# Performance work log

Hardware: AMD Instinct MI355X
Metric: run time of the kernel (lower is better)

## Reference

```python
import jax, jax.numpy as jnp
import numpy as np

N = 50000      # num nodes
NE = 20000     # num hyperedges
NNZ = 1000000  # incidence pairs |{(v,e)}|
F_IN = 128
HID = 64
NCLS = 40
NLAYER = 4
ALPHA = 0.1    # args.restart_alpha
LAMDA = 0.5


def setup_inputs() -> dict:
    key = jax.random.key(0)
    ks = jax.random.split(key, 8)
    x = jax.random.normal(ks[0], (N, F_IN), dtype=jnp.float32)
    vertex = jax.random.randint(ks[1], (NNZ,), 0, N, dtype=jnp.int32)
    edges = jax.random.randint(ks[2], (NNZ,), 0, NE, dtype=jnp.int32)
    W0 = jax.random.normal(ks[3], (F_IN, HID), dtype=jnp.float32) / np.float32(np.sqrt(F_IN))
    b0 = jnp.zeros((HID,), jnp.float32)
    Ws = jax.random.normal(ks[4], (NLAYER, HID, HID), dtype=jnp.float32) / np.float32(np.sqrt(HID))
    Wout = jax.random.normal(ks[5], (HID, NCLS), dtype=jnp.float32) / np.float32(np.sqrt(HID))
    bout = jnp.zeros((NCLS,), jnp.float32)
    return {"x": x, "vertex": vertex, "edges": edges, "W0": W0, "b0": b0,
            "Ws": Ws, "Wout": Wout, "bout": bout}


def _scatter_mean(src, idx, num_segments):
    s = jax.ops.segment_sum(src, idx, num_segments=num_segments)
    cnt = jax.ops.segment_sum(jnp.ones((idx.shape[0],), src.dtype), idx, num_segments=num_segments)
    return s / jnp.maximum(cnt, 1.0)[:, None]


def _normalize_l2(X):
    # torch: rownorm = X.detach().norm(dim=1, keepdim=True); scale = rownorm^-1; inf->0
    norm = jax.lax.stop_gradient(jnp.sqrt(jnp.sum(X * X, axis=-1, keepdims=True)))
    scale = jnp.where(norm > 0, 1.0 / jnp.maximum(norm, jnp.float32(1e-30)), 0.0)
    return X * scale


def reference(x, vertex, edges, W0, b0, Ws, Wout, bout):
    # input linear + relu (dropout = identity in eval mode)
    X = jax.nn.relu(x @ W0 + b0)
    X0 = X
    for i in range(NLAYER):
        beta = float(np.log(LAMDA / (i + 1) + 1.0))
        Xve = X[vertex]                       # gather node -> incidence  [NNZ, HID]
        Xe = _scatter_mean(Xve, edges, NE)    # scatter-mean -> hyperedge [NE, HID]
        Xev = Xe[edges]                       # gather hyperedge -> incidence [NNZ, HID]
        Xv = _scatter_mean(Xev, vertex, N)    # scatter-mean -> node      [N, HID]
        Xv = _normalize_l2(Xv)                # args.UniGNN_use_norm = True
        Xi = (1.0 - ALPHA) * Xv + ALPHA * X0
        X = jax.nn.relu((1.0 - beta) * Xi + beta * (Xi @ Ws[i]))
    return X @ Wout + bout
```

## Files before the change

### kernel.cpp

```cpp
#include <hip/hip_runtime.h>
#include <hip/hip_fp16.h>
#include <math.h>

#define N_NODES 50000
#define N_EDGES 20000
#define NNZ_C   1000000
#define F_IN    128
#define HID     64
#define NCLS    40
#define NLAYER  4
#define ALPHA   0.1f

#define ESHIFT  6
#define VSHIFT  7
#define NB_E    ((N_EDGES + 63) / 64)
#define NB_V    ((N_NODES + 127) / 128)
#define NB_TOT  (NB_E + NB_V)

typedef _Float16 f16x8 __attribute__((ext_vector_type(8)));
typedef float    f32x4 __attribute__((ext_vector_type(4)));

__global__ __launch_bounds__(256) void input_gemm(
    const float* __restrict__ x, const float* __restrict__ W0,
    const float* __restrict__ b0, _Float16* __restrict__ X0h)
{
    int lane = threadIdx.x & 63;
    int wv   = threadIdx.x >> 6;
    int r16  = lane & 15;
    int kgrp = lane >> 4;
    f16x8 bf[4][4];
    #pragma unroll
    for (int n0 = 0; n0 < 4; ++n0)
        #pragma unroll
        for (int kh = 0; kh < 4; ++kh)
            #pragma unroll
            for (int j = 0; j < 8; ++j)
                bf[n0][kh][j] = (_Float16)W0[(kh * 32 + kgrp * 8 + j) * HID + n0 * 16 + r16];
    float bias[4];
    #pragma unroll
    for (int n0 = 0; n0 < 4; ++n0) bias[n0] = b0[n0 * 16 + r16];

    int nwaves = gridDim.x * 4;
    for (int t = blockIdx.x * 4 + wv; t < N_NODES / 16; t += nwaves) {
        int row0 = t * 16;
        const float* xp = x + (size_t)(row0 + r16) * F_IN + kgrp * 8;
        f16x8 a[4];
        #pragma unroll
        for (int kh = 0; kh < 4; ++kh) {
            float4 u0 = *(const float4*)(xp + kh * 32);
            float4 u1 = *(const float4*)(xp + kh * 32 + 4);
            a[kh][0] = (_Float16)u0.x; a[kh][1] = (_Float16)u0.y;
            a[kh][2] = (_Float16)u0.z; a[kh][3] = (_Float16)u0.w;
            a[kh][4] = (_Float16)u1.x; a[kh][5] = (_Float16)u1.y;
            a[kh][6] = (_Float16)u1.z; a[kh][7] = (_Float16)u1.w;
        }
        #pragma unroll
        for (int n0 = 0; n0 < 4; ++n0) {
            f32x4 acc = {0.f, 0.f, 0.f, 0.f};
            #pragma unroll
            for (int kh = 0; kh < 4; ++kh)
                acc = __builtin_amdgcn_mfma_f32_16x16x32_f16(a[kh], bf[n0][kh], acc, 0, 0, 0);
            #pragma unroll
            for (int r = 0; r < 4; ++r) {
                float y = acc[r] + bias[n0];
                y = y > 0.f ? y : 0.f;
                X0h[(size_t)(row0 + kgrp * 4 + r) * HID + n0 * 16 + r16] = (_Float16)y;
            }
        }
    }
}

__global__ __launch_bounds__(256) void make_wp(
    const float* __restrict__ Ws, _Float16* __restrict__ Wp,
    float be0, float be1, float be2, float be3)
{
    int l = blockIdx.x;
    float beta = (l == 0) ? be0 : (l == 1) ? be1 : (l == 2) ? be2 : be3;
    for (int i = threadIdx.x; i < HID * HID; i += 256) {
        int k = i >> 6, n = i & 63;
        float v = beta * Ws[l * HID * HID + i] + ((k == n) ? (1.f - beta) : 0.f);
        Wp[l * HID * HID + i] = (_Float16)v;
    }
}

__global__ __launch_bounds__(256) void bucket_hist(
    const int* __restrict__ vertex, const int* __restrict__ edges,
    int* __restrict__ gcnt)
{
    __shared__ int h[NB_TOT];
    int tid = threadIdx.x;
    for (int i = tid; i < NB_TOT; i += 256) h[i] = 0;
    __syncthreads();
    int base = blockIdx.x * 4096;
    int n = NNZ_C - base; if (n > 4096) n = 4096;
    for (int i = tid * 4; i < n; i += 1024) {
        int4 e4 = *(const int4*)(edges  + base + i);
        int4 v4 = *(const int4*)(vertex + base + i);
        atomicAdd(&h[e4.x >> ESHIFT], 1);
        atomicAdd(&h[e4.y >> ESHIFT], 1);
        atomicAdd(&h[e4.z >> ESHIFT], 1);
        atomicAdd(&h[e4.w >> ESHIFT], 1);
        atomicAdd(&h[NB_E + (v4.x >> VSHIFT)], 1);
        atomicAdd(&h[NB_E + (v4.y >> VSHIFT)], 1);
        atomicAdd(&h[NB_E + (v4.z >> VSHIFT)], 1);
        atomicAdd(&h[NB_E + (v4.w >> VSHIFT)], 1);
    }
    __syncthreads();
    for (int i = tid; i < NB_TOT; i += 256)
        if (h[i]) atomicAdd(&gcnt[i], h[i]);
}

__global__ __launch_bounds__(1024) void bucket_scan(
    const int* __restrict__ gcnt, int* __restrict__ boff_e,
    int* __restrict__ boff_v, int* __restrict__ curb)
{
    __shared__ int tmp[1024];
    int tid = threadIdx.x;
    int v = (tid < NB_TOT) ? gcnt[tid] : 0;
    tmp[tid] = v;
    __syncthreads();
    for (int d = 1; d < 1024; d <<= 1) {
        int t = (tid >= d) ? tmp[tid - d] : 0;
        __syncthreads();
        tmp[tid] += t;
        __syncthreads();
    }
    if (tid < NB_TOT) {
        int excl = tmp[tid] - v;
        int off = (tid < NB_E) ? excl : excl - NNZ_C;
        if (tid < NB_E) boff_e[tid] = off; else boff_v[tid - NB_E] = off;
        curb[tid] = off;
    }
    if (tid == 0) { boff_e[NB_E] = NNZ_C; boff_v[NB_V] = NNZ_C; }
}

__global__ __launch_bounds__(256) void bin_pass1_both(
    const int* __restrict__ vertex, const int* __restrict__ edges,
    int* __restrict__ curb,
    unsigned* __restrict__ binned_e,
    unsigned* __restrict__ binned_v)
{
    __shared__ int hist[NB_TOT];
    __shared__ int base[NB_TOT];
    int tid = threadIdx.x;
    int blk = blockIdx.x * 4096;
    int nh = NNZ_C - blk; if (nh > 4096) nh = 4096;
    int ee[16], vv[16];
    int nche = 0;
    #pragma unroll
    for (int k = 0; k < 4; ++k) {
        int i = tid * 4 + k * 1024;
        if (i < nh) {
            int4 e4 = *(const int4*)(edges  + blk + i);
            int4 v4 = *(const int4*)(vertex + blk + i);
            ee[k*4+0]=e4.x; ee[k*4+1]=e4.y; ee[k*4+2]=e4.z; ee[k*4+3]=e4.w;
            vv[k*4+0]=v4.x; vv[k*4+1]=v4.y; vv[k*4+2]=v4.z; vv[k*4+3]=v4.w;
            nche = k + 1;
        }
    }
    for (int i = tid; i < NB_TOT; i += 256) hist[i] = 0;
    __syncthreads();
    for (int k = 0; k < nche; ++k) {
        #pragma unroll
        for (int q = 0; q < 4; ++q) {
            atomicAdd(&hist[ee[k*4+q] >> ESHIFT], 1);
            atomicAdd(&hist[NB_E + (vv[k*4+q] >> VSHIFT)], 1);
        }
    }
    __syncthreads();
    for (int i = tid; i < NB_TOT; i += 256) {
        int c = hist[i];
        base[i] = c ? atomicAdd(&curb[i], c) : 0;
        hist[i] = 0;
    }
    __syncthreads();
    for (int k = 0; k < nche; ++k) {
        #pragma unroll
        for (int q = 0; q < 4; ++q) {
            int e = ee[k*4+q], v = vv[k*4+q];
            int be = e >> ESHIFT;
            int r  = atomicAdd(&hist[be], 1);
            binned_e[base[be] + r] = ((unsigned)e << 16) | (unsigned)v;
            int bv = NB_E + (v >> VSHIFT);
            int r2 = atomicAdd(&hist[bv], 1);
            binned_v[base[bv] + r2] = ((unsigned)v << 15) | (unsigned)e;
        }
    }
}

__global__ __launch_bounds__(256) void bin_pass2f(
    const unsigned* __restrict__ binned, const int* __restrict__ boff,
    int shift, int kshift, int nkeys,
    int* __restrict__ off, float* __restrict__ inv, int* __restrict__ adj)
{
    __shared__ int lcnt[128];
    __shared__ int ts[128];
    __shared__ int lcur[128];
    int b  = blockIdx.x;
    int k0 = b << shift;
    int bs = 1 << shift;
    int kn = nkeys - k0; if (kn > bs) kn = bs;
    int tid = threadIdx.x;
    unsigned vmask = (1u << kshift) - 1u;
    if (tid < 128) lcnt[tid] = 0;
    __syncthreads();
    int beg = boff[b], end = boff[b + 1];
    for (int j = beg + tid; j < end; j += 256)
        atomicAdd(&lcnt[(int)(binned[j] >> kshift) - k0], 1);
    __syncthreads();
    int c = 0;
    if (tid < 128) { c = lcnt[tid]; ts[tid] = c; }
    __syncthreads();
    #pragma unroll
    for (int d = 1; d < 128; d <<= 1) {
        int t = 0;
        if (tid < 128 && tid >= d) t = ts[tid - d];
        __syncthreads();
        if (tid < 128) ts[tid] += t;
        __syncthreads();
    }
    if (tid < kn) {
        int pos = beg + ts[tid] - c;
        off[k0 + tid] = pos;
        inv[k0 + tid] = 1.0f / fmaxf((float)c, 1.0f);
        lcur[tid] = pos;
    }
    if (b == 0 && tid == 0) off[nkeys] = NNZ_C;
    __syncthreads();
    for (int j = beg + tid; j < end; j += 256) {
        unsigned p = binned[j];
        int k = (int)(p >> kshift) - k0;
        int v = (int)(p & vmask);
        adj[atomicAdd(&lcur[k], 1)] = v;
    }
}

__device__ __forceinline__ void gather_rows(
    const __half* __restrict__ src, const int* __restrict__ adj,
    int beg, int end, int lane, float acc[8])
{
    int g = lane >> 3, c = lane & 7;
    for (int j = beg; j < end; j += 64) {
        int nj = end - j; if (nj > 64) nj = 64;
        int myidx = (lane < nj) ? adj[j + lane] : 0;
        int idx[8];
        #pragma unroll
        for (int s = 0; s < 8; ++s)
            idx[s] = __shfl(myidx, ((s << 3) + g) & 63);
        #pragma unroll
        for (int s = 0; s < 8; ++s) {
            int r = (s << 3) + g;
            if (r < nj) {
                uint4 raw = ((const uint4*)(src + (size_t)idx[s] * HID))[c];
                union { uint4 u; __half2 h[4]; } U; U.u = raw;
                float2 f0 = __half22float2(U.h[0]);
                float2 f1 = __half22float2(U.h[1]);
                float2 f2 = __half22float2(U.h[2]);
                float2 f3 = __half22float2(U.h[3]);
                acc[0] += f0.x; acc[1] += f0.y;
                acc[2] += f1.x; acc[3] += f1.y;
                acc[4] += f2.x; acc[5] += f2.y;
                acc[6] += f3.x; acc[7] += f3.y;
            }
        }
    }
    #pragma unroll
    for (int q = 0; q < 8; ++q) {
        acc[q] += __shfl_xor(acc[q], 8);
        acc[q] += __shfl_xor(acc[q], 16);
        acc[q] += __shfl_xor(acc[q], 32);
    }
}

__global__ __launch_bounds__(256) void edge_gather(
    const __half* __restrict__ Xh, const int* __restrict__ adj_e,
    const int* __restrict__ off_e, const float* __restrict__ inv_e,
    __half* __restrict__ Xeh)
{
    int wid  = blockIdx.x * 4 + (threadIdx.x >> 6);
    int lane = threadIdx.x & 63;
    float acc[8] = {0.f,0.f,0.f,0.f,0.f,0.f,0.f,0.f};
    gather_rows(Xh, adj_e, off_e[wid], off_e[wid + 1], lane, acc);
    if ((lane >> 3) == 0) {
        float sc = inv_e[wid];
        union { uint4 u; __half2 h[4]; } O;
        O.h[0] = __floats2half2_rn(acc[0] * sc, acc[1] * sc);
        O.h[1] = __floats2half2_rn(acc[2] * sc, acc[3] * sc);
        O.h[2] = __floats2half2_rn(acc[4] * sc, acc[5] * sc);
        O.h[3] = __floats2half2_rn(acc[6] * sc, acc[7] * sc);
        ((uint4*)(Xeh + (size_t)wid * HID))[lane] = O.u;
    }
}

__global__ __launch_bounds__(256) void node_gather(
    const __half* __restrict__ Xeh, const int* __restrict__ adj_v,
    const int* __restrict__ off_v, const float* __restrict__ inv_v,
    const _Float16* __restrict__ X0h, _Float16* __restrict__ Xi)
{
    int wv   = threadIdx.x >> 6;
    int row  = blockIdx.x * 4 + wv;
    int lane = threadIdx.x & 63;
    float acc[8] = {0.f,0.f,0.f,0.f,0.f,0.f,0.f,0.f};
    gather_rows(Xeh, adj_v, off_v[row], off_v[row + 1], lane, acc);
    float scm = inv_v[row];
    float m[8]; float s = 0.f;
    #pragma unroll
    for (int q = 0; q < 8; ++q) { m[q] = acc[q] * scm; s += m[q] * m[q]; }
    s += __shfl_xor(s, 1);
    s += __shfl_xor(s, 2);
    s += __shfl_xor(s, 4);
    float norm  = sqrtf(s);
    float scale = norm > 0.f ? 1.0f / norm : 0.f;
    if ((lane >> 3) == 0) {
        union { f16x8 v; uint4 u; } I;
        I.u = *(const uint4*)(X0h + (size_t)row * HID + lane * 8);
        union { f16x8 v; uint4 u; } O;
        #pragma unroll
        for (int q = 0; q < 8; ++q)
            O.v[q] = (_Float16)((1.0f - ALPHA) * (m[q] * scale) + ALPHA * (float)I.v[q]);
        *(uint4*)(Xi + (size_t)row * HID + lane * 8) = O.u;
    }
}

__global__ __launch_bounds__(256) void layer_gemm(
    const _Float16* __restrict__ Xi, const _Float16* __restrict__ Wp,
    _Float16* __restrict__ Xh)
{
    int lane = threadIdx.x & 63;
    int wv   = threadIdx.x >> 6;
    int r16  = lane & 15;
    int kgrp = lane >> 4;
    f16x8 bf[4][2];
    #pragma unroll
    for (int n0 = 0; n0 < 4; ++n0)
        #pragma unroll
        for (int kh = 0; kh < 2; ++kh) {
            #pragma unroll
            for (int j = 0; j < 8; ++j)
                bf[n0][kh][j] = Wp[(kh * 32 + kgrp * 8 + j) * HID + n0 * 16 + r16];
        }
    int nwaves = gridDim.x * 4;
    for (int t = blockIdx.x * 4 + wv; t < N_NODES / 16; t += nwaves) {
        int row0 = t * 16;
        const _Float16* ap = Xi + (size_t)(row0 + r16) * HID + kgrp * 8;
        f16x8 a0 = *(const f16x8*)(ap);
        f16x8 a1 = *(const f16x8*)(ap + 32);
        #pragma unroll
        for (int n0 = 0; n0 < 4; ++n0) {
            f32x4 acc = {0.f, 0.f, 0.f, 0.f};
            acc = __builtin_amdgcn_mfma_f32_16x16x32_f16(a0, bf[n0][0], acc, 0, 0, 0);
            acc = __builtin_amdgcn_mfma_f32_16x16x32_f16(a1, bf[n0][1], acc, 0, 0, 0);
            #pragma unroll
            for (int r = 0; r < 4; ++r) {
                float y = acc[r] > 0.f ? acc[r] : 0.f;
                Xh[(size_t)(row0 + kgrp * 4 + r) * HID + n0 * 16 + r16] = (_Float16)y;
            }
        }
    }
}

__global__ __launch_bounds__(256) void out_gemm(
    const _Float16* __restrict__ Xh, const float* __restrict__ Wout,
    const float* __restrict__ bout, float* __restrict__ out)
{
    int lane = threadIdx.x & 63;
    int wv   = threadIdx.x >> 6;
    int r16  = lane & 15;
    int kgrp = lane >> 4;
    f16x8 bf[3][2];
    float bias[3];
    #pragma unroll
    for (int n0 = 0; n0 < 3; ++n0) {
        int col = n0 * 16 + r16;
        bias[n0] = (col < NCLS) ? bout[col] : 0.f;
        #pragma unroll
        for (int kh = 0; kh < 2; ++kh)
            #pragma unroll
            for (int j = 0; j < 8; ++j) {
                int k = kh * 32 + kgrp * 8 + j;
                bf[n0][kh][j] = (col < NCLS) ? (_Float16)Wout[k * NCLS + col] : (_Float16)0.f;
            }
    }
    int nwaves = gridDim.x * 4;
    for (int t = blockIdx.x * 4 + wv; t < N_NODES / 16; t += nwaves) {
        int row0 = t * 16;
        const _Float16* ap = Xh + (size_t)(row0 + r16) * HID + kgrp * 8;
        f16x8 a0 = *(const f16x8*)(ap);
        f16x8 a1 = *(const f16x8*)(ap + 32);
        #pragma unroll
        for (int n0 = 0; n0 < 3; ++n0) {
            f32x4 acc = {0.f, 0.f, 0.f, 0.f};
            acc = __builtin_amdgcn_mfma_f32_16x16x32_f16(a0, bf[n0][0], acc, 0, 0, 0);
            acc = __builtin_amdgcn_mfma_f32_16x16x32_f16(a1, bf[n0][1], acc, 0, 0, 0);
            int col = n0 * 16 + r16;
            if (col < NCLS) {
                #pragma unroll
                for (int r = 0; r < 4; ++r)
                    out[(size_t)(row0 + kgrp * 4 + r) * NCLS + col] = acc[r] + bias[n0];
            }
        }
    }
}

extern "C" void kernel_launch(void* const* d_in, const int* in_sizes, int n_in,
                              void* d_out, int out_size, void* d_ws, size_t ws_size,
                              hipStream_t stream)
{
    const float* x      = (const float*)d_in[0];
    const int*   vertex = (const int*)  d_in[1];
    const int*   edges  = (const int*)  d_in[2];
    const float* W0     = (const float*)d_in[3];
    const float* b0     = (const float*)d_in[4];
    const float* Ws     = (const float*)d_in[5];
    const float* Wout   = (const float*)d_in[6];
    const float* bout   = (const float*)d_in[7];
    float* out = (float*)d_out;

    char* ws = (char*)d_ws;
    unsigned* binned_e = (unsigned*)ws; ws += (size_t)NNZ_C * 4;
    unsigned* binned_v = (unsigned*)ws; ws += (size_t)NNZ_C * 4;
    _Float16*  X0h  = (_Float16*)ws;  ws += (size_t)N_NODES * HID * 2;
    _Float16*  Xh   = (_Float16*)ws;  ws += (size_t)N_NODES * HID * 2;
    _Float16*  Xi   = (_Float16*)ws;  ws += (size_t)N_NODES * HID * 2;
    __half*    Xeh  = (__half*)ws;    ws += (size_t)N_EDGES * HID * 2;
    _Float16*  Wp   = (_Float16*)ws;  ws += (size_t)NLAYER * HID * HID * 2;
    int*   adj_e  = (int*)ws;     ws += (size_t)NNZ_C * 4;
    int*   adj_v  = (int*)ws;     ws += (size_t)NNZ_C * 4;
    int*   off_e  = (int*)ws;     ws += (size_t)(N_EDGES + 1) * 4;
    int*   off_v  = (int*)ws;     ws += (size_t)(N_NODES + 1) * 4;
    float* inv_e  = (float*)ws;   ws += (size_t)N_EDGES * 4;
    float* inv_v  = (float*)ws;   ws += (size_t)N_NODES * 4;
    int*   gcnt   = (int*)ws;     ws += (size_t)NB_TOT * 4;
    int*   boff_e = (int*)ws;     ws += (size_t)(NB_E + 1) * 4;
    int*   boff_v = (int*)ws;     ws += (size_t)(NB_V + 1) * 4;
    int*   curb   = (int*)ws;     ws += (size_t)NB_TOT * 4;

    const int p1_grid = (NNZ_C + 4095) / 4096;

    hipMemsetAsync(gcnt, 0, (size_t)NB_TOT * 4, stream);
    bucket_hist<<<p1_grid, 256, 0, stream>>>(vertex, edges, gcnt);
    bucket_scan<<<1, 1024, 0, stream>>>(gcnt, boff_e, boff_v, curb);
    bin_pass1_both<<<p1_grid, 256, 0, stream>>>(vertex, edges, curb, binned_e, binned_v);
    bin_pass2f<<<NB_E, 256, 0, stream>>>(binned_e, boff_e, ESHIFT, 16, N_EDGES, off_e, inv_e, adj_e);
    bin_pass2f<<<NB_V, 256, 0, stream>>>(binned_v, boff_v, VSHIFT, 15, N_NODES, off_v, inv_v, adj_v);

    float be0 = logf(0.5f / 1.f + 1.0f);
    float be1 = logf(0.5f / 2.f + 1.0f);
    float be2 = logf(0.5f / 3.f + 1.0f);
    float be3 = logf(0.5f / 4.f + 1.0f);
    make_wp<<<NLAYER, 256, 0, stream>>>(Ws, Wp, be0, be1, be2, be3);

    input_gemm<<<391, 256, 0, stream>>>(x, W0, b0, X0h);

    for (int l = 0; l < NLAYER; ++l) {
        const _Float16* Xin = (l == 0) ? X0h : Xh;
        edge_gather<<<N_EDGES / 4, 256, 0, stream>>>((const __half*)Xin, adj_e, off_e, inv_e, Xeh);
        node_gather<<<N_NODES / 4, 256, 0, stream>>>(
            Xeh, adj_v, off_v, inv_v, X0h, Xi);
        layer_gemm<<<391, 256, 0, stream>>>(Xi, Wp + (size_t)l * HID * HID, Xh);
    }

    out_gemm<<<391, 256, 0, stream>>>(Xh, Wout, bout, out);
}
```

Measured before the change: 282.4 us.

## Process two nodes per wave in node_gather and merge bin_pass2 launches

node_gather now assigns two consecutive node rows to each wavefront and interleaves their gathers, so each wave has twice as many independent loads in flight and the grid is halved. Nodes average about 20 incidences, so the old one-row-per-wave scheme left most lanes of a 64-wide chunk idle. The two bin_pass2f launches are merged into one grid that picks the edge or vertex side by block index, saving a launch and letting both sides run at once. In exchange the node kernel uses more registers and loops until the longer of the two rows is done.

```diff
diff --git a/kernel.cpp b/kernel.cpp
--- a/kernel.cpp
+++ b/kernel.cpp
@@ -188,15 +188,26 @@
     }
 }
 
-__global__ __launch_bounds__(256) void bin_pass2f(
-    const unsigned* __restrict__ binned, const int* __restrict__ boff,
-    int shift, int kshift, int nkeys,
-    int* __restrict__ off, float* __restrict__ inv, int* __restrict__ adj)
-{
+__global__ __launch_bounds__(256) void bin_pass2_both(
+    const unsigned* __restrict__ binned_e, const unsigned* __restrict__ binned_v,
+    const int* __restrict__ boff_e, const int* __restrict__ boff_v,
+    int* __restrict__ off_e, float* __restrict__ inv_e, int* __restrict__ adj_e,
+    int* __restrict__ off_v, float* __restrict__ inv_v, int* __restrict__ adj_v)
+{
+    bool is_e = blockIdx.x < NB_E;
+    const unsigned* binned = is_e ? binned_e : binned_v;
+    const int*      boff   = is_e ? boff_e   : boff_v;
+    int*   off = is_e ? off_e : off_v;
+    float* inv = is_e ? inv_e : inv_v;
+    int*   adj = is_e ? adj_e : adj_v;
+    int b      = is_e ? blockIdx.x : blockIdx.x - NB_E;
+    int shift  = is_e ? ESHIFT : VSHIFT;
+    int kshift = is_e ? 16 : 15;
+    int nkeys  = is_e ? N_EDGES : N_NODES;
+
     __shared__ int lcnt[128];
     __shared__ int ts[128];
     __shared__ int lcur[128];
-    int b  = blockIdx.x;
     int k0 = b << shift;
     int bs = 1 << shift;
     int kn = nkeys - k0; if (kn > bs) kn = bs;
@@ -272,6 +283,16 @@
     }
 }
 
+__device__ __forceinline__ void reduce_groups(float acc[8])
+{
+    #pragma unroll
+    for (int q = 0; q < 8; ++q) {
+        acc[q] += __shfl_xor(acc[q], 8);
+        acc[q] += __shfl_xor(acc[q], 16);
+        acc[q] += __shfl_xor(acc[q], 32);
+    }
+}
+
 __global__ __launch_bounds__(256) void edge_gather(
     const __half* __restrict__ Xh, const int* __restrict__ adj_e,
     const int* __restrict__ off_e, const float* __restrict__ inv_e,
@@ -298,27 +319,84 @@
     const _Float16* __restrict__ X0h, _Float16* __restrict__ Xi)
 {
     int wv   = threadIdx.x >> 6;
-    int row  = blockIdx.x * 4 + wv;
+    int pr   = blockIdx.x * 4 + wv;
     int lane = threadIdx.x & 63;
-    float acc[8] = {0.f,0.f,0.f,0.f,0.f,0.f,0.f,0.f};
-    gather_rows(Xeh, adj_v, off_v[row], off_v[row + 1], lane, acc);
-    float scm = inv_v[row];
-    float m[8]; float s = 0.f;
-    #pragma unroll
-    for (int q = 0; q < 8; ++q) { m[q] = acc[q] * scm; s += m[q] * m[q]; }
-    s += __shfl_xor(s, 1);
-    s += __shfl_xor(s, 2);
-    s += __shfl_xor(s, 4);
-    float norm  = sqrtf(s);
-    float scale = norm > 0.f ? 1.0f / norm : 0.f;
-    if ((lane >> 3) == 0) {
-        union { f16x8 v; uint4 u; } I;
-        I.u = *(const uint4*)(X0h + (size_t)row * HID + lane * 8);
-        union { f16x8 v; uint4 u; } O;
-        #pragma unroll
-        for (int q = 0; q < 8; ++q)
-            O.v[q] = (_Float16)((1.0f - ALPHA) * (m[q] * scale) + ALPHA * (float)I.v[q]);
-        *(uint4*)(Xi + (size_t)row * HID + lane * 8) = O.u;
+    int rowA = pr * 2, rowB = rowA + 1;
+    int begA = off_v[rowA];
+    int endA = off_v[rowA + 1];
+    int endB = off_v[rowB + 1];
+    int begB = endA;
+    int g = lane >> 3, c = lane & 7;
+    float accA[8] = {0.f,0.f,0.f,0.f,0.f,0.f,0.f,0.f};
+    float accB[8] = {0.f,0.f,0.f,0.f,0.f,0.f,0.f,0.f};
+    int jA = begA, jB = begB;
+    while (jA < endA || jB < endB) {
+        int njA = endA - jA; njA = njA < 0 ? 0 : (njA > 64 ? 64 : njA);
+        int njB = endB - jB; njB = njB < 0 ? 0 : (njB > 64 ? 64 : njB);
+        int mA = (lane < njA) ? adj_v[jA + lane] : 0;
+        int mB = (lane < njB) ? adj_v[jB + lane] : 0;
+        int iA[8], iB[8];
+        #pragma unroll
+        for (int s = 0; s < 8; ++s) {
+            iA[s] = __shfl(mA, ((s << 3) + g) & 63);
+            iB[s] = __shfl(mB, ((s << 3) + g) & 63);
+        }
+        #pragma unroll
+        for (int s = 0; s < 8; ++s) {
+            int r = (s << 3) + g;
+            if (r < njA) {
+                uint4 raw = ((const uint4*)(Xeh + (size_t)iA[s] * HID))[c];
+                union { uint4 u; __half2 h[4]; } U; U.u = raw;
+                float2 f0 = __half22float2(U.h[0]);
+                float2 f1 = __half22float2(U.h[1]);
+                float2 f2 = __half22float2(U.h[2]);
+                float2 f3 = __half22float2(U.h[3]);
+                accA[0] += f0.x; accA[1] += f0.y;
+                accA[2] += f1.x; accA[3] += f1.y;
+                accA[4] += f2.x; accA[5] += f2.y;
+                accA[6] += f3.x; accA[7] += f3.y;
+            }
+            if (r < njB) {
+                uint4 raw = ((const uint4*)(Xeh + (size_t)iB[s] * HID))[c];
+                union { uint4 u; __half2 h[4]; } U; U.u = raw;
+                float2 f0 = __half22float2(U.h[0]);
+                float2 f1 = __half22float2(U.h[1]);
+                float2 f2 = __half22float2(U.h[2]);
+                float2 f3 = __half22float2(U.h[3]);
+                accB[0] += f0.x; accB[1] += f0.y;
+                accB[2] += f1.x; accB[3] += f1.y;
+                accB[4] += f2.x; accB[5] += f2.y;
+                accB[6] += f3.x; accB[7] += f3.y;
+            }
+        }
+        jA += 64; jB += 64;
+    }
+    reduce_groups(accA);
+    reduce_groups(accB);
+    float scmA = inv_v[rowA], scmB = inv_v[rowB];
+    float mAv[8], mBv[8];
+    float sA = 0.f, sB = 0.f;
+    #pragma unroll
+    for (int q = 0; q < 8; ++q) {
+        mAv[q] = accA[q] * scmA; sA += mAv[q] * mAv[q];
+        mBv[q] = accB[q] * scmB; sB += mBv[q] * mBv[q];
+    }
+    sA += __shfl_xor(sA, 1); sA += __shfl_xor(sA, 2); sA += __shfl_xor(sA, 4);
+    sB += __shfl_xor(sB, 1); sB += __shfl_xor(sB, 2); sB += __shfl_xor(sB, 4);
+    float nA = sqrtf(sA), nB = sqrtf(sB);
+    float scaleA = nA > 0.f ? 1.0f / nA : 0.f;
+    float scaleB = nB > 0.f ? 1.0f / nB : 0.f;
+    if (g < 2) {
+        int   row   = g ? rowB : rowA;
+        float scale = g ? scaleB : scaleA;
+        union { f16x8 v; uint4 u; } I, O;
+        I.u = *(const uint4*)(X0h + (size_t)row * HID + c * 8);
+        #pragma unroll
+        for (int q = 0; q < 8; ++q) {
+            float mv = g ? mBv[q] : mAv[q];
+            O.v[q] = (_Float16)((1.0f - ALPHA) * (mv * scale) + ALPHA * (float)I.v[q]);
+        }
+        *(uint4*)(Xi + (size_t)row * HID + c * 8) = O.u;
     }
 }
 
@@ -441,8 +519,9 @@
     bucket_hist<<<p1_grid, 256, 0, stream>>>(vertex, edges, gcnt);
     bucket_scan<<<1, 1024, 0, stream>>>(gcnt, boff_e, boff_v, curb);
     bin_pass1_both<<<p1_grid, 256, 0, stream>>>(vertex, edges, curb, binned_e, binned_v);
-    bin_pass2f<<<NB_E, 256, 0, stream>>>(binned_e, boff_e, ESHIFT, 16, N_EDGES, off_e, inv_e, adj_e);
-    bin_pass2f<<<NB_V, 256, 0, stream>>>(binned_v, boff_v, VSHIFT, 15, N_NODES, off_v, inv_v, adj_v);
+    bin_pass2_both<<<NB_TOT, 256, 0, stream>>>(binned_e, binned_v, boff_e, boff_v,
+                                               off_e, inv_e, adj_e,
+                                               off_v, inv_v, adj_v);
 
     float be0 = logf(0.5f / 1.f + 1.0f);
     float be1 = logf(0.5f / 2.f + 1.0f);
@@ -455,7 +534,7 @@
     for (int l = 0; l < NLAYER; ++l) {
         const _Float16* Xin = (l == 0) ? X0h : Xh;
         edge_gather<<<N_EDGES / 4, 256, 0, stream>>>((const __half*)Xin, adj_e, off_e, inv_e, Xeh);
-        node_gather<<<N_NODES / 4, 256, 0, stream>>>(
+        node_gather<<<N_NODES / 8, 256, 0, stream>>>(
             Xeh, adj_v, off_v, inv_v, X0h, Xi);
         layer_gemm<<<391, 256, 0, stream>>>(Xi, Wp + (size_t)l * HID * HID, Xh);
     }
```

New measurement: 287.9 us. About the same (+1.9%).
